# Optimization experiments

Measured on AMD Instinct MI355X. Metric: run time of the kernel, lower is better.

Reference implementation:

```python
import jax, jax.numpy as jnp
import numpy as np

NUM_HEAD = 8
HEAD_DIM = 32
MAX_DIST = 128
RATIO = 4  # smooth_embedding_ratio


def setup_inputs() -> dict:
    key = jax.random.key(0)
    ks = jax.random.split(key, 8)
    B, L, C = 4, 2048, 64
    H, D, md = NUM_HEAD, HEAD_DIM, MAX_DIST
    Wsm = (2 * md + 1) // RATIO  # 64

    def g(k, shape, scale=0.05):
        return jax.random.normal(k, shape, dtype=jnp.float32) * scale

    return {
        "x": g(ks[0], (B, L, C), 1.0),
        "Wq": g(ks[1], (C, H * D)),
        "bq": jnp.zeros((H * D,), jnp.float32),
        "Wk": g(ks[2], (C, H * D)),
        "bk": jnp.zeros((H * D,), jnp.float32),
        "Wv": g(ks[3], (C, H)),
        "distance_pe": g(ks[4], (H, D, Wsm, 1)),
        "u_pe": g(ks[5], (H, 1, 1, D)),
        "v_pe": g(ks[6], (H, 1, 1, D)),
    }


def reference(x, Wq, bq, Wk, bk, Wv, distance_pe, u_pe, v_pe):
    H, D, md = NUM_HEAD, HEAD_DIM, MAX_DIST
    W = 2 * md + 1
    B, L, _ = x.shape

    # projections, split into heads: (H, B, L, D)
    q = (x @ Wq + bq).reshape(B, L, H, D).transpose(2, 0, 1, 3)
    k = (x @ Wk + bk).reshape(B, L, H, D).transpose(2, 0, 1, 3)
    v = jax.nn.sigmoid(x @ Wv).transpose(2, 0, 1)  # (H, B, L)

    # Banded (q+u) @ k^T without materializing the full LxL score matrix.
    # TF does matmul + diag_part(k=(-md, md)) + permute + double reverse, which
    # equals att[h,b,n,m] = <q_u[h,b,(L-1-n)-(m-md)], k[h,b,L-1-n]> (0 if OOB).
    q_u = q + u_pe  # (H, B, L, D)
    q_pad = jnp.pad(q_u, ((0, 0), (0, 0), (md, md), (0, 0)))  # zeros match diag_part padding

    def band_at(m):
        # q_pad[j + 2*md - m] == q_u[j - (m - md)] (zero when out of range)
        qs = jax.lax.dynamic_slice_in_dim(q_pad, 2 * md - m, L, axis=2)
        return jnp.einsum('hbld,hbld->hbl', qs, k)

    band = jax.lax.map(band_at, jnp.arange(W))  # (W, H, B, L)
    att = jnp.transpose(band, (1, 2, 3, 0))[:, :, ::-1, :]  # (H, B, L, W)

    # Smoothed distance PE: bilinear upsample width Wsm -> W (TF2 half-pixel centers)
    smooth_pe = jax.image.resize(distance_pe, (H, D, W, 1), method='linear')[..., 0]  # (H, D, W)
    att = att + jnp.einsum('hbld,hdw->hblw', q + v_pe, smooth_pe)

    att = jax.nn.softmax(att * (float(D) ** -0.5), axis=-1)
    att = att * v[..., None]  # sigmoid value gating

    out = att.sum(axis=2)  # global mode: reduce over data_length -> (H, B, W)
    return jnp.transpose(out, (1, 2, 0))  # (B, W, H)
```

## Files before the change

kernel.cpp:

```cpp
#include <hip/hip_runtime.h>
#include <math.h>

#define NH 8
#define HD 32
#define MD 128
#define NW 257
#define NWP 272
#define WSM 64
#define NB 4
#define NL 2048
#define NC 64
#define NHD 256
#define SP 40
#define ROWS 128
#define WIN 384
#define WTS 72
#define TRS 136
#define SC2 0.2550928063161107f

#define NBLK 512

using bf16x8 = __attribute__((ext_vector_type(8))) short;
using f32x4  = __attribute__((ext_vector_type(4))) float;
using i32x4  = __attribute__((ext_vector_type(4))) int;

__device__ __forceinline__ unsigned cvtpk(float lo, float hi) {
  unsigned r;
  asm("v_cvt_pk_bf16_f32 %0, %1, %2" : "=v"(r) : "v"(lo), "v"(hi));
  return r;
}
__device__ __forceinline__ unsigned short f2b(float f) {
  return (unsigned short)cvtpk(f, f);
}
__device__ __forceinline__ void stb(unsigned short* p, float f) {
  *p = f2b(f);
}

__global__ __launch_bounds__(512, 4) void phaseA_kernel(
    const float* __restrict__ x,
    const float* __restrict__ Wq, const float* __restrict__ bq,
    const float* __restrict__ Wk, const float* __restrict__ bk,
    const float* __restrict__ Wv, const float* __restrict__ dpe,
    const float* __restrict__ u_pe,
    unsigned short* __restrict__ qu,
    unsigned short* __restrict__ kb, float* __restrict__ vv,
    unsigned short* __restrict__ spt, float* __restrict__ out) {
  __shared__ __align__(16) unsigned short wt[128 * WTS];
  __shared__ __align__(16) unsigned short tr[64 * TRS];
  const int bid = blockIdx.x;
  const int tid = threadIdx.x;

  bf16x8 a0, a1;
  int c = 0, g = 0, g8 = 0, w = 0, b = 0, l0 = 0, cb = 0;
  bool isQ = true;

  if (tid < 256) {
    const int t = tid;
    const int l64 = t & 63;
    w = t >> 6;
    c = l64 & 15; g = l64 >> 4; g8 = g * 8;
    const int br = bid >> 2;
    const int c0 = (bid & 3) << 7;
    const int r0 = br << 6;
    b = r0 >> 11;
    l0 = r0 & (NL - 1);
    isQ = (c0 < 256);
    const float* Wsrc = isQ ? Wq : Wk;
    cb = isQ ? c0 : c0 - 256;

#pragma unroll
    for (int i = 0; i < 4; ++i) {
      const int flat = t + i * 256;
      const int col4 = flat & 31;
      const int kp = flat >> 5;
      const float4 w0 = *reinterpret_cast<const float4*>(Wsrc + (2 * kp) * NHD + cb + 4 * col4);
      const float4 w1 = *reinterpret_cast<const float4*>(Wsrc + (2 * kp + 1) * NHD + cb + 4 * col4);
      unsigned* wp = reinterpret_cast<unsigned*>(wt);
      wp[(4 * col4 + 0) * (WTS / 2) + kp] = cvtpk(w0.x, w1.x);
      wp[(4 * col4 + 1) * (WTS / 2) + kp] = cvtpk(w0.y, w1.y);
      wp[(4 * col4 + 2) * (WTS / 2) + kp] = cvtpk(w0.z, w1.z);
      wp[(4 * col4 + 3) * (WTS / 2) + kp] = cvtpk(w0.w, w1.w);
    }

    const float* xr = x + (size_t)(r0 + 16 * w + c) * NC;
    const float4 x00 = *reinterpret_cast<const float4*>(xr + g8);
    const float4 x01 = *reinterpret_cast<const float4*>(xr + g8 + 4);
    const float4 x10 = *reinterpret_cast<const float4*>(xr + 32 + g8);
    const float4 x11 = *reinterpret_cast<const float4*>(xr + 32 + g8 + 4);
    const i32x4 a0i = {(int)cvtpk(x00.x, x00.y), (int)cvtpk(x00.z, x00.w),
                       (int)cvtpk(x01.x, x01.y), (int)cvtpk(x01.z, x01.w)};
    const i32x4 a1i = {(int)cvtpk(x10.x, x10.y), (int)cvtpk(x10.z, x10.w),
                       (int)cvtpk(x11.x, x11.y), (int)cvtpk(x11.z, x11.w)};
    a0 = __builtin_bit_cast(bf16x8, a0i);
    a1 = __builtin_bit_cast(bf16x8, a1i);
  } else if (tid < 384) {
    const int k = tid - 256;
    const int j = k >> 3, hh = k & 7;
    const int row = bid * 16 + j;
    const float* xr = x + (size_t)row * NC;
    float a = 0.f;
#pragma unroll
    for (int c4 = 0; c4 < NC / 4; ++c4) {
      const float4 xv = *reinterpret_cast<const float4*>(xr + 4 * c4);
      a = fmaf(xv.x, Wv[(4 * c4 + 0) * NH + hh], a);
      a = fmaf(xv.y, Wv[(4 * c4 + 1) * NH + hh], a);
      a = fmaf(xv.z, Wv[(4 * c4 + 2) * NH + hh], a);
      a = fmaf(xv.w, Wv[(4 * c4 + 3) * NH + hh], a);
    }
    const int bb = row >> 11, ll = row & (NL - 1);
    vv[((size_t)hh * NB + bb) * NL + ll] = 1.f / (1.f + __expf(-a));
  } else {
    const int k = tid - 384;
    if (k < 17) {
      const int oz = bid * 17 + k;
      if (oz < NB * NW * NH) out[oz] = 0.f;
    }
#pragma unroll
    for (int it = 0; it < 2; ++it) {
      const int k2 = k + it * 128;
      const int idx = bid * 136 + k2;
      if (k2 < 136 && idx < NH * NWP * HD) {
        const int d = idx & 31;
        const int hm = idx >> 5;
        const int m = hm % NWP;
        const int h = hm / NWP;
        float val = 0.f;
        if (m < NW) {
          float tt = (m + 0.5f) * ((float)WSM / (float)NW) - 0.5f;
          tt = fminf(fmaxf(tt, 0.f), (float)(WSM - 1));
          const int i0 = (int)tt;
          const float f = tt - (float)i0;
          const int i1 = (i0 + 1 < WSM) ? i0 + 1 : WSM - 1;
          const float* bse = dpe + ((size_t)h * HD + d) * WSM;
          val = (bse[i0] * (1.f - f) + bse[i1] * f) * SC2;
        }
        stb(spt + idx, val);
      }
    }
  }

  __syncthreads();

  if (tid < 256) {
    f32x4 acc[8];
#pragma unroll
    for (int tt = 0; tt < 8; ++tt) acc[tt] = {0.f, 0.f, 0.f, 0.f};
    __builtin_amdgcn_s_setprio(1);
#pragma unroll
    for (int tt = 0; tt < 8; ++tt) {
      const bf16x8 b0 = *reinterpret_cast<const bf16x8*>(&wt[(16 * tt + c) * WTS + g8]);
      const bf16x8 b1 = *reinterpret_cast<const bf16x8*>(&wt[(16 * tt + c) * WTS + 32 + g8]);
      acc[tt] = __builtin_amdgcn_mfma_f32_16x16x32_bf16(a0, b0, acc[tt], 0, 0, 0);
      acc[tt] = __builtin_amdgcn_mfma_f32_16x16x32_bf16(a1, b1, acc[tt], 0, 0, 0);
    }
    __builtin_amdgcn_s_setprio(0);
#pragma unroll
    for (int tt = 0; tt < 8; ++tt) {
      const int col = cb + 16 * tt + c;
      const float bias = isQ ? (bq[col] + u_pe[col]) : bk[col];
#pragma unroll
      for (int r = 0; r < 4; ++r) {
        const float val = isQ ? (acc[tt][r] + bias) : ((acc[tt][r] + bias) * SC2);
        tr[(16 * w + 4 * g + r) * TRS + 16 * tt + c] = f2b(val);
      }
    }
  }

  __syncthreads();

  if (tid < 256) {
    unsigned short* dst = isQ ? qu : kb;
#pragma unroll
    for (int i = 0; i < 4; ++i) {
      const int idx = tid + i * 256;
      const int row = idx >> 4;
      const int hd4 = (idx >> 2) & 3;
      const int ch = idx & 3;
      const i32x4 v = *reinterpret_cast<const i32x4*>(&tr[row * TRS + hd4 * 32 + ch * 8]);
      const int col0 = cb + hd4 * 32;
      const int h = col0 >> 5;
      *reinterpret_cast<i32x4*>(dst + (((size_t)h * NB + b) * NL + l0 + row) * HD + ch * 8) = v;
    }
  }
}

__global__ __launch_bounds__(512, 4) void phaseB_kernel(
    const unsigned short* __restrict__ qu,
    const unsigned short* __restrict__ kb, const float* __restrict__ vv,
    const unsigned short* __restrict__ spt,
    const float* __restrict__ u_pe, const float* __restrict__ v_pe,
    float* __restrict__ out) {
  __shared__ __align__(16) unsigned short qu_sh[WIN * SP];
  float* red = reinterpret_cast<float*>(qu_sh);

  const int raw = blockIdx.x;
  const int bid = (raw & 7) * 64 + (raw >> 3);
  const int tid = threadIdx.x;

  const int tile = bid & 15;
  const int hb = bid >> 4;
  const int b = hb & (NB - 1);
  const int h = hb >> 2;
  const int hc0 = h * HD;
  const int n0 = tile << 7;
  const int jlo = NL - ROWS - n0;
  const int l = tid & 63;
  const int w = tid >> 6;
  const int c = l & 15;
  const int g = l >> 4;
  const int g8 = g * 8;

  const unsigned short* qu_h = qu + (size_t)hb * NL * HD;
  const unsigned short* k_h  = kb + (size_t)hb * NL * HD;
  const unsigned short* sp_h = spt + (size_t)h * NWP * HD;
  const float* vv_h = vv + (size_t)hb * NL;

  const bf16x8 ak = *reinterpret_cast<const bf16x8*>(k_h + (size_t)(jlo + 16 * w + c) * HD + g8);
  const i32x4 qraw = *reinterpret_cast<const i32x4*>(qu_h + (size_t)(n0 + 127 - 16 * w - c) * HD + g8);
  const f32x4 v4 = *reinterpret_cast<const f32x4*>(vv_h + (n0 + 124 - 16 * w - 4 * g));

  const int wq0_blk = jlo - MD;
  i32x4 stq[3];
#pragma unroll
  for (int it = 0; it < 3; ++it) {
    const int p = tid + it * 512;
    const int gr = wq0_blk + (p >> 2);
    i32x4 val = {0, 0, 0, 0};
    if ((unsigned)gr < (unsigned)NL)
      val = *reinterpret_cast<const i32x4*>(qu_h + (size_t)gr * HD + (p & 3) * 8);
    stq[it] = val;
  }

  const float4 u0 = *reinterpret_cast<const float4*>(u_pe + hc0 + g8);
  const float4 u1 = *reinterpret_cast<const float4*>(u_pe + hc0 + g8 + 4);
  const float4 v0 = *reinterpret_cast<const float4*>(v_pe + hc0 + g8);
  const float4 v1 = *reinterpret_cast<const float4*>(v_pe + hc0 + g8 + 4);
  const float duv[8] = {v0.x - u0.x, v0.y - u0.y, v0.z - u0.z, v0.w - u0.w,
                        v1.x - u1.x, v1.y - u1.y, v1.z - u1.z, v1.w - u1.w};
  i32x4 aqv_i;
#pragma unroll
  for (int k2 = 0; k2 < 4; ++k2) {
    const unsigned uq = (unsigned)qraw[k2];
    const float lo = __builtin_bit_cast(float, uq << 16) + duv[2 * k2];
    const float hi = __builtin_bit_cast(float, uq & 0xffff0000u) + duv[2 * k2 + 1];
    aqv_i[k2] = (int)cvtpk(lo, hi);
  }
  const bf16x8 aqv = __builtin_bit_cast(bf16x8, aqv_i);

  const f32x4 z4 = {0.f, 0.f, 0.f, 0.f};

  f32x4 s[17];
  __builtin_amdgcn_s_setprio(1);
#pragma unroll
  for (int t = 0; t < 17; ++t) {
    const bf16x8 bsp = *reinterpret_cast<const bf16x8*>(sp_h + (size_t)(16 * t + c) * HD + g8);
    s[t] = __builtin_amdgcn_mfma_f32_16x16x32_bf16(aqv, bsp, z4, 0, 0, 0);
  }
  __builtin_amdgcn_s_setprio(0);

#pragma unroll
  for (int it = 0; it < 3; ++it) {
    const int p = tid + it * 512;
    *reinterpret_cast<i32x4*>(&qu_sh[(p >> 2) * SP + (p & 3) * 8]) = stq[it];
  }
  __syncthreads();

  int sl[4]; bool cond[4];
#pragma unroll
  for (int r = 0; r < 4; ++r) {
    sl[r] = 16 * g + ((4 * g + r - c) & 15);
    cond[r] = (4 * g + r) >= c;
  }

  f32x4 shp;
  __builtin_amdgcn_s_setprio(1);
#pragma unroll
  for (int U = 0; U <= 16; ++U) {
    const bf16x8 bqu = *reinterpret_cast<const bf16x8*>(&qu_sh[(16 * w + 16 * U + c) * SP + g8]);
    const f32x4 c1 = __builtin_amdgcn_mfma_f32_16x16x32_bf16(ak, bqu, z4, 0, 0, 0);
    f32x4 shc;
#pragma unroll
    for (int r = 0; r < 4; ++r) shc[r] = __shfl(c1[r], sl[r], 64);
    if (U == 0) {
#pragma unroll
      for (int r = 0; r < 4; ++r)
        s[16][r] = (c == 0) ? (s[16][r] + shc[r]) : -1e30f;
    } else {
#pragma unroll
      for (int r = 0; r < 4; ++r)
        s[16 - U][r] += cond[r] ? shc[r] : shp[r];
    }
    shp = shc;
  }
  __builtin_amdgcn_s_setprio(0);

  float wgt[4];
#pragma unroll
  for (int r = 0; r < 4; ++r) {
    float sum = 0.f;
#pragma unroll
    for (int t = 0; t < 17; ++t) {
      const float p = exp2f(s[t][r]);
      s[t][r] = p;
      sum += p;
    }
#pragma unroll
    for (int off = 1; off < 16; off <<= 1) sum += __shfl_xor(sum, off, 16);
    wgt[r] = v4[3 - r] * __builtin_amdgcn_rcpf(sum);
  }

  __syncthreads();
#pragma unroll
  for (int t = 0; t < 17; ++t) {
    float y = s[t][0] * wgt[0] + s[t][1] * wgt[1] + s[t][2] * wgt[2] + s[t][3] * wgt[3];
    y += __shfl_xor(y, 16, 64);
    y += __shfl_xor(y, 32, 64);
    if (l < 16) red[w * NWP + 16 * t + c] = y;
  }
  __syncthreads();
  for (int m = tid; m < NW; m += 512) {
    float ssum = 0.f;
#pragma unroll
    for (int ww = 0; ww < 8; ++ww) ssum += red[ww * NWP + m];
    atomicAdd(&out[((size_t)b * NW + m) * NH + h], ssum);
  }
}

extern "C" void kernel_launch(void* const* d_in, const int* in_sizes, int n_in,
                              void* d_out, int out_size, void* d_ws, size_t ws_size,
                              hipStream_t stream) {
  const float* x = (const float*)d_in[0];
  const float* Wq = (const float*)d_in[1];
  const float* bq = (const float*)d_in[2];
  const float* Wk = (const float*)d_in[3];
  const float* bk = (const float*)d_in[4];
  const float* Wv = (const float*)d_in[5];
  const float* dpe = (const float*)d_in[6];
  const float* u_pe = (const float*)d_in[7];
  const float* v_pe = (const float*)d_in[8];
  float* out = (float*)d_out;

  const size_t qk_elems = (size_t)NH * NB * NL * HD;
  float* vv = (float*)d_ws;
  unsigned short* qu = (unsigned short*)(vv + (size_t)NH * NB * NL);
  unsigned short* kb = qu + qk_elems;
  unsigned short* spt = kb + qk_elems;

  hipLaunchKernelGGL(phaseA_kernel, dim3(NBLK), dim3(512), 0, stream,
                     x, Wq, bq, Wk, bk, Wv, dpe, u_pe, qu, kb, vv, spt, out);
  hipLaunchKernelGGL(phaseB_kernel, dim3(NBLK), dim3(512), 0, stream,
                     qu, kb, vv, spt, u_pe, v_pe, out);
}
```

Measured before the change: 31.70 us.

## Fuse projection and band-attention phases into one kernel with grid barrier

Merges the two kernels into a single kernel. An atomic-counter grid-wide barrier separates the projection phase from the banded attention phase, and shared memory is aliased between the phases. This removes the second kernel launch and the gap between kernels. In exchange it adds a memset to reset the counter, and it relies on all 512 blocks being co-resident, or the spin barrier deadlocks.

After: 110.7 us. +249.1%, slower.

```diff
diff --git a/kernel.cpp b/kernel.cpp
--- a/kernel.cpp
+++ b/kernel.cpp
@@ -19,6 +19,7 @@
 #define SC2 0.2550928063161107f
 
 #define NBLK 512
+#define SMEM_U16 17920
 
 using bf16x8 = __attribute__((ext_vector_type(8))) short;
 using f32x4  = __attribute__((ext_vector_type(4))) float;
@@ -36,293 +37,301 @@
   *p = f2b(f);
 }
 
-__global__ __launch_bounds__(512, 4) void phaseA_kernel(
+__global__ __launch_bounds__(512, 4) void fused_kernel(
     const float* __restrict__ x,
     const float* __restrict__ Wq, const float* __restrict__ bq,
     const float* __restrict__ Wk, const float* __restrict__ bk,
     const float* __restrict__ Wv, const float* __restrict__ dpe,
-    const float* __restrict__ u_pe,
+    const float* __restrict__ u_pe, const float* __restrict__ v_pe,
     unsigned short* __restrict__ qu,
     unsigned short* __restrict__ kb, float* __restrict__ vv,
-    unsigned short* __restrict__ spt, float* __restrict__ out) {
-  __shared__ __align__(16) unsigned short wt[128 * WTS];
-  __shared__ __align__(16) unsigned short tr[64 * TRS];
-  const int bid = blockIdx.x;
+    unsigned short* __restrict__ spt, unsigned* __restrict__ ctr,
+    float* __restrict__ out) {
+  __shared__ __align__(16) unsigned short smem[SMEM_U16];
+  unsigned short* wt = smem;
+  unsigned short* tr = smem + 128 * WTS;
+  unsigned short* qu_sh = smem;
+  float* red = reinterpret_cast<float*>(smem);
+
+  const int rawbid = blockIdx.x;
   const int tid = threadIdx.x;
 
-  bf16x8 a0, a1;
-  int c = 0, g = 0, g8 = 0, w = 0, b = 0, l0 = 0, cb = 0;
-  bool isQ = true;
-
-  if (tid < 256) {
-    const int t = tid;
-    const int l64 = t & 63;
-    w = t >> 6;
-    c = l64 & 15; g = l64 >> 4; g8 = g * 8;
-    const int br = bid >> 2;
-    const int c0 = (bid & 3) << 7;
-    const int r0 = br << 6;
-    b = r0 >> 11;
-    l0 = r0 & (NL - 1);
-    isQ = (c0 < 256);
-    const float* Wsrc = isQ ? Wq : Wk;
-    cb = isQ ? c0 : c0 - 256;
-
-#pragma unroll
-    for (int i = 0; i < 4; ++i) {
-      const int flat = t + i * 256;
-      const int col4 = flat & 31;
-      const int kp = flat >> 5;
-      const float4 w0 = *reinterpret_cast<const float4*>(Wsrc + (2 * kp) * NHD + cb + 4 * col4);
-      const float4 w1 = *reinterpret_cast<const float4*>(Wsrc + (2 * kp + 1) * NHD + cb + 4 * col4);
-      unsigned* wp = reinterpret_cast<unsigned*>(wt);
-      wp[(4 * col4 + 0) * (WTS / 2) + kp] = cvtpk(w0.x, w1.x);
-      wp[(4 * col4 + 1) * (WTS / 2) + kp] = cvtpk(w0.y, w1.y);
-      wp[(4 * col4 + 2) * (WTS / 2) + kp] = cvtpk(w0.z, w1.z);
-      wp[(4 * col4 + 3) * (WTS / 2) + kp] = cvtpk(w0.w, w1.w);
-    }
-
-    const float* xr = x + (size_t)(r0 + 16 * w + c) * NC;
-    const float4 x00 = *reinterpret_cast<const float4*>(xr + g8);
-    const float4 x01 = *reinterpret_cast<const float4*>(xr + g8 + 4);
-    const float4 x10 = *reinterpret_cast<const float4*>(xr + 32 + g8);
-    const float4 x11 = *reinterpret_cast<const float4*>(xr + 32 + g8 + 4);
-    const i32x4 a0i = {(int)cvtpk(x00.x, x00.y), (int)cvtpk(x00.z, x00.w),
-                       (int)cvtpk(x01.x, x01.y), (int)cvtpk(x01.z, x01.w)};
-    const i32x4 a1i = {(int)cvtpk(x10.x, x10.y), (int)cvtpk(x10.z, x10.w),
-                       (int)cvtpk(x11.x, x11.y), (int)cvtpk(x11.z, x11.w)};
-    a0 = __builtin_bit_cast(bf16x8, a0i);
-    a1 = __builtin_bit_cast(bf16x8, a1i);
-  } else if (tid < 384) {
-    const int k = tid - 256;
-    const int j = k >> 3, hh = k & 7;
-    const int row = bid * 16 + j;
-    const float* xr = x + (size_t)row * NC;
-    float a = 0.f;
-#pragma unroll
-    for (int c4 = 0; c4 < NC / 4; ++c4) {
-      const float4 xv = *reinterpret_cast<const float4*>(xr + 4 * c4);
-      a = fmaf(xv.x, Wv[(4 * c4 + 0) * NH + hh], a);
-      a = fmaf(xv.y, Wv[(4 * c4 + 1) * NH + hh], a);
-      a = fmaf(xv.z, Wv[(4 * c4 + 2) * NH + hh], a);
-      a = fmaf(xv.w, Wv[(4 * c4 + 3) * NH + hh], a);
-    }
-    const int bb = row >> 11, ll = row & (NL - 1);
-    vv[((size_t)hh * NB + bb) * NL + ll] = 1.f / (1.f + __expf(-a));
-  } else {
-    const int k = tid - 384;
-    if (k < 17) {
-      const int oz = bid * 17 + k;
-      if (oz < NB * NW * NH) out[oz] = 0.f;
-    }
-#pragma unroll
-    for (int it = 0; it < 2; ++it) {
-      const int k2 = k + it * 128;
-      const int idx = bid * 136 + k2;
-      if (k2 < 136 && idx < NH * NWP * HD) {
-        const int d = idx & 31;
-        const int hm = idx >> 5;
-        const int m = hm % NWP;
-        const int h = hm / NWP;
-        float val = 0.f;
-        if (m < NW) {
-          float tt = (m + 0.5f) * ((float)WSM / (float)NW) - 0.5f;
-          tt = fminf(fmaxf(tt, 0.f), (float)(WSM - 1));
-          const int i0 = (int)tt;
-          const float f = tt - (float)i0;
-          const int i1 = (i0 + 1 < WSM) ? i0 + 1 : WSM - 1;
-          const float* bse = dpe + ((size_t)h * HD + d) * WSM;
-          val = (bse[i0] * (1.f - f) + bse[i1] * f) * SC2;
+  {
+    const int bid = rawbid;
+    bf16x8 a0, a1;
+    int c = 0, g = 0, g8 = 0, w = 0, b = 0, l0 = 0, cb = 0;
+    bool isQ = true;
+
+    if (tid < 256) {
+      const int t = tid;
+      const int l64 = t & 63;
+      w = t >> 6;
+      c = l64 & 15; g = l64 >> 4; g8 = g * 8;
+      const int br = bid >> 2;
+      const int c0 = (bid & 3) << 7;
+      const int r0 = br << 6;
+      b = r0 >> 11;
+      l0 = r0 & (NL - 1);
+      isQ = (c0 < 256);
+      const float* Wsrc = isQ ? Wq : Wk;
+      cb = isQ ? c0 : c0 - 256;
+
+#pragma unroll
+      for (int i = 0; i < 4; ++i) {
+        const int flat = t + i * 256;
+        const int col4 = flat & 31;
+        const int kp = flat >> 5;
+        const float4 w0 = *reinterpret_cast<const float4*>(Wsrc + (2 * kp) * NHD + cb + 4 * col4);
+        const float4 w1 = *reinterpret_cast<const float4*>(Wsrc + (2 * kp + 1) * NHD + cb + 4 * col4);
+        unsigned* wp = reinterpret_cast<unsigned*>(wt);
+        wp[(4 * col4 + 0) * (WTS / 2) + kp] = cvtpk(w0.x, w1.x);
+        wp[(4 * col4 + 1) * (WTS / 2) + kp] = cvtpk(w0.y, w1.y);
+        wp[(4 * col4 + 2) * (WTS / 2) + kp] = cvtpk(w0.z, w1.z);
+        wp[(4 * col4 + 3) * (WTS / 2) + kp] = cvtpk(w0.w, w1.w);
+      }
+
+      const float* xr = x + (size_t)(r0 + 16 * w + c) * NC;
+      const float4 x00 = *reinterpret_cast<const float4*>(xr + g8);
+      const float4 x01 = *reinterpret_cast<const float4*>(xr + g8 + 4);
+      const float4 x10 = *reinterpret_cast<const float4*>(xr + 32 + g8);
+      const float4 x11 = *reinterpret_cast<const float4*>(xr + 32 + g8 + 4);
+      const i32x4 a0i = {(int)cvtpk(x00.x, x00.y), (int)cvtpk(x00.z, x00.w),
+                         (int)cvtpk(x01.x, x01.y), (int)cvtpk(x01.z, x01.w)};
+      const i32x4 a1i = {(int)cvtpk(x10.x, x10.y), (int)cvtpk(x10.z, x10.w),
+                         (int)cvtpk(x11.x, x11.y), (int)cvtpk(x11.z, x11.w)};
+      a0 = __builtin_bit_cast(bf16x8, a0i);
+      a1 = __builtin_bit_cast(bf16x8, a1i);
+    } else if (tid < 384) {
+      const int k = tid - 256;
+      const int j = k >> 3, hh = k & 7;
+      const int row = bid * 16 + j;
+      const float* xr = x + (size_t)row * NC;
+      float a = 0.f;
+#pragma unroll
+      for (int c4 = 0; c4 < NC / 4; ++c4) {
+        const float4 xv = *reinterpret_cast<const float4*>(xr + 4 * c4);
+        a = fmaf(xv.x, Wv[(4 * c4 + 0) * NH + hh], a);
+        a = fmaf(xv.y, Wv[(4 * c4 + 1) * NH + hh], a);
+        a = fmaf(xv.z, Wv[(4 * c4 + 2) * NH + hh], a);
+        a = fmaf(xv.w, Wv[(4 * c4 + 3) * NH + hh], a);
+      }
+      const int bb = row >> 11, ll = row & (NL - 1);
+      vv[((size_t)hh * NB + bb) * NL + ll] = 1.f / (1.f + __expf(-a));
+    } else {
+      const int k = tid - 384;
+      if (k < 17) {
+        const int oz = bid * 17 + k;
+        if (oz < NB * NW * NH) out[oz] = 0.f;
+      }
+#pragma unroll
+      for (int it = 0; it < 2; ++it) {
+        const int k2 = k + it * 128;
+        const int idx = bid * 136 + k2;
+        if (k2 < 136 && idx < NH * NWP * HD) {
+          const int d = idx & 31;
+          const int hm = idx >> 5;
+          const int m = hm % NWP;
+          const int h = hm / NWP;
+          float val = 0.f;
+          if (m < NW) {
+            float tt = (m + 0.5f) * ((float)WSM / (float)NW) - 0.5f;
+            tt = fminf(fmaxf(tt, 0.f), (float)(WSM - 1));
+            const int i0 = (int)tt;
+            const float f = tt - (float)i0;
+            const int i1 = (i0 + 1 < WSM) ? i0 + 1 : WSM - 1;
+            const float* bse = dpe + ((size_t)h * HD + d) * WSM;
+            val = (bse[i0] * (1.f - f) + bse[i1] * f) * SC2;
+          }
+          stb(spt + idx, val);
         }
-        stb(spt + idx, val);
+      }
+    }
+
+    __syncthreads();
+
+    if (tid < 256) {
+      f32x4 acc[8];
+#pragma unroll
+      for (int tt = 0; tt < 8; ++tt) acc[tt] = {0.f, 0.f, 0.f, 0.f};
+      __builtin_amdgcn_s_setprio(1);
+#pragma unroll
+      for (int tt = 0; tt < 8; ++tt) {
+        const bf16x8 b0 = *reinterpret_cast<const bf16x8*>(&wt[(16 * tt + c) * WTS + g8]);
+        const bf16x8 b1 = *reinterpret_cast<const bf16x8*>(&wt[(16 * tt + c) * WTS + 32 + g8]);
+        acc[tt] = __builtin_amdgcn_mfma_f32_16x16x32_bf16(a0, b0, acc[tt], 0, 0, 0);
+        acc[tt] = __builtin_amdgcn_mfma_f32_16x16x32_bf16(a1, b1, acc[tt], 0, 0, 0);
+      }
+      __builtin_amdgcn_s_setprio(0);
+#pragma unroll
+      for (int tt = 0; tt < 8; ++tt) {
+        const int col = cb + 16 * tt + c;
+        const float bias = isQ ? (bq[col] + u_pe[col]) : bk[col];
+#pragma unroll
+        for (int r = 0; r < 4; ++r) {
+          const float val = isQ ? (acc[tt][r] + bias) : ((acc[tt][r] + bias) * SC2);
+          tr[(16 * w + 4 * g + r) * TRS + 16 * tt + c] = f2b(val);
+        }
+      }
+    }
+
+    __syncthreads();
+
+    if (tid < 256) {
+      unsigned short* dst = isQ ? qu : kb;
+#pragma unroll
+      for (int i = 0; i < 4; ++i) {
+        const int idx = tid + i * 256;
+        const int row = idx >> 4;
+        const int hd4 = (idx >> 2) & 3;
+        const int ch = idx & 3;
+        const i32x4 v = *reinterpret_cast<const i32x4*>(&tr[row * TRS + hd4 * 32 + ch * 8]);
+        const int col0 = cb + hd4 * 32;
+        const int h = col0 >> 5;
+        *reinterpret_cast<i32x4*>(dst + (((size_t)h * NB + b) * NL + l0 + row) * HD + ch * 8) = v;
       }
     }
   }
 
   __syncthreads();
-
-  if (tid < 256) {
-    f32x4 acc[8];
-#pragma unroll
-    for (int tt = 0; tt < 8; ++tt) acc[tt] = {0.f, 0.f, 0.f, 0.f};
-    __builtin_amdgcn_s_setprio(1);
-#pragma unroll
-    for (int tt = 0; tt < 8; ++tt) {
-      const bf16x8 b0 = *reinterpret_cast<const bf16x8*>(&wt[(16 * tt + c) * WTS + g8]);
-      const bf16x8 b1 = *reinterpret_cast<const bf16x8*>(&wt[(16 * tt + c) * WTS + 32 + g8]);
-      acc[tt] = __builtin_amdgcn_mfma_f32_16x16x32_bf16(a0, b0, acc[tt], 0, 0, 0);
-      acc[tt] = __builtin_amdgcn_mfma_f32_16x16x32_bf16(a1, b1, acc[tt], 0, 0, 0);
-    }
-    __builtin_amdgcn_s_setprio(0);
-#pragma unroll
-    for (int tt = 0; tt < 8; ++tt) {
-      const int col = cb + 16 * tt + c;
-      const float bias = isQ ? (bq[col] + u_pe[col]) : bk[col];
-#pragma unroll
-      for (int r = 0; r < 4; ++r) {
-        const float val = isQ ? (acc[tt][r] + bias) : ((acc[tt][r] + bias) * SC2);
-        tr[(16 * w + 4 * g + r) * TRS + 16 * tt + c] = f2b(val);
-      }
-    }
-  }
-
-  __syncthreads();
-
-  if (tid < 256) {
-    unsigned short* dst = isQ ? qu : kb;
-#pragma unroll
-    for (int i = 0; i < 4; ++i) {
-      const int idx = tid + i * 256;
-      const int row = idx >> 4;
-      const int hd4 = (idx >> 2) & 3;
-      const int ch = idx & 3;
-      const i32x4 v = *reinterpret_cast<const i32x4*>(&tr[row * TRS + hd4 * 32 + ch * 8]);
-      const int col0 = cb + hd4 * 32;
-      const int h = col0 >> 5;
-      *reinterpret_cast<i32x4*>(dst + (((size_t)h * NB + b) * NL + l0 + row) * HD + ch * 8) = v;
-    }
-  }
-}
-
-__global__ __launch_bounds__(512, 4) void phaseB_kernel(
-    const unsigned short* __restrict__ qu,
-    const unsigned short* __restrict__ kb, const float* __restrict__ vv,
-    const unsigned short* __restrict__ spt,
-    const float* __restrict__ u_pe, const float* __restrict__ v_pe,
-    float* __restrict__ out) {
-  __shared__ __align__(16) unsigned short qu_sh[WIN * SP];
-  float* red = reinterpret_cast<float*>(qu_sh);
-
-  const int raw = blockIdx.x;
-  const int bid = (raw & 7) * 64 + (raw >> 3);
-  const int tid = threadIdx.x;
-
-  const int tile = bid & 15;
-  const int hb = bid >> 4;
-  const int b = hb & (NB - 1);
-  const int h = hb >> 2;
-  const int hc0 = h * HD;
-  const int n0 = tile << 7;
-  const int jlo = NL - ROWS - n0;
-  const int l = tid & 63;
-  const int w = tid >> 6;
-  const int c = l & 15;
-  const int g = l >> 4;
-  const int g8 = g * 8;
-
-  const unsigned short* qu_h = qu + (size_t)hb * NL * HD;
-  const unsigned short* k_h  = kb + (size_t)hb * NL * HD;
-  const unsigned short* sp_h = spt + (size_t)h * NWP * HD;
-  const float* vv_h = vv + (size_t)hb * NL;
-
-  const bf16x8 ak = *reinterpret_cast<const bf16x8*>(k_h + (size_t)(jlo + 16 * w + c) * HD + g8);
-  const i32x4 qraw = *reinterpret_cast<const i32x4*>(qu_h + (size_t)(n0 + 127 - 16 * w - c) * HD + g8);
-  const f32x4 v4 = *reinterpret_cast<const f32x4*>(vv_h + (n0 + 124 - 16 * w - 4 * g));
-
-  const int wq0_blk = jlo - MD;
-  i32x4 stq[3];
-#pragma unroll
-  for (int it = 0; it < 3; ++it) {
-    const int p = tid + it * 512;
-    const int gr = wq0_blk + (p >> 2);
-    i32x4 val = {0, 0, 0, 0};
-    if ((unsigned)gr < (unsigned)NL)
-      val = *reinterpret_cast<const i32x4*>(qu_h + (size_t)gr * HD + (p & 3) * 8);
-    stq[it] = val;
-  }
-
-  const float4 u0 = *reinterpret_cast<const float4*>(u_pe + hc0 + g8);
-  const float4 u1 = *reinterpret_cast<const float4*>(u_pe + hc0 + g8 + 4);
-  const float4 v0 = *reinterpret_cast<const float4*>(v_pe + hc0 + g8);
-  const float4 v1 = *reinterpret_cast<const float4*>(v_pe + hc0 + g8 + 4);
-  const float duv[8] = {v0.x - u0.x, v0.y - u0.y, v0.z - u0.z, v0.w - u0.w,
-                        v1.x - u1.x, v1.y - u1.y, v1.z - u1.z, v1.w - u1.w};
-  i32x4 aqv_i;
-#pragma unroll
-  for (int k2 = 0; k2 < 4; ++k2) {
-    const unsigned uq = (unsigned)qraw[k2];
-    const float lo = __builtin_bit_cast(float, uq << 16) + duv[2 * k2];
-    const float hi = __builtin_bit_cast(float, uq & 0xffff0000u) + duv[2 * k2 + 1];
-    aqv_i[k2] = (int)cvtpk(lo, hi);
-  }
-  const bf16x8 aqv = __builtin_bit_cast(bf16x8, aqv_i);
-
-  const f32x4 z4 = {0.f, 0.f, 0.f, 0.f};
-
-  f32x4 s[17];
-  __builtin_amdgcn_s_setprio(1);
-#pragma unroll
-  for (int t = 0; t < 17; ++t) {
-    const bf16x8 bsp = *reinterpret_cast<const bf16x8*>(sp_h + (size_t)(16 * t + c) * HD + g8);
-    s[t] = __builtin_amdgcn_mfma_f32_16x16x32_bf16(aqv, bsp, z4, 0, 0, 0);
-  }
-  __builtin_amdgcn_s_setprio(0);
-
-#pragma unroll
-  for (int it = 0; it < 3; ++it) {
-    const int p = tid + it * 512;
-    *reinterpret_cast<i32x4*>(&qu_sh[(p >> 2) * SP + (p & 3) * 8]) = stq[it];
+  if (tid == 0) {
+    __threadfence();
+    __hip_atomic_fetch_add(ctr, 1u, __ATOMIC_ACQ_REL, __HIP_MEMORY_SCOPE_AGENT);
+    while (__hip_atomic_load(ctr, __ATOMIC_ACQUIRE, __HIP_MEMORY_SCOPE_AGENT) < (unsigned)NBLK)
+      __builtin_amdgcn_s_sleep(8);
+    __threadfence();
   }
   __syncthreads();
 
-  int sl[4]; bool cond[4];
-#pragma unroll
-  for (int r = 0; r < 4; ++r) {
-    sl[r] = 16 * g + ((4 * g + r - c) & 15);
-    cond[r] = (4 * g + r) >= c;
-  }
-
-  f32x4 shp;
-  __builtin_amdgcn_s_setprio(1);
-#pragma unroll
-  for (int U = 0; U <= 16; ++U) {
-    const bf16x8 bqu = *reinterpret_cast<const bf16x8*>(&qu_sh[(16 * w + 16 * U + c) * SP + g8]);
-    const f32x4 c1 = __builtin_amdgcn_mfma_f32_16x16x32_bf16(ak, bqu, z4, 0, 0, 0);
-    f32x4 shc;
-#pragma unroll
-    for (int r = 0; r < 4; ++r) shc[r] = __shfl(c1[r], sl[r], 64);
-    if (U == 0) {
-#pragma unroll
-      for (int r = 0; r < 4; ++r)
-        s[16][r] = (c == 0) ? (s[16][r] + shc[r]) : -1e30f;
-    } else {
-#pragma unroll
-      for (int r = 0; r < 4; ++r)
-        s[16 - U][r] += cond[r] ? shc[r] : shp[r];
-    }
-    shp = shc;
-  }
-  __builtin_amdgcn_s_setprio(0);
-
-  float wgt[4];
-#pragma unroll
-  for (int r = 0; r < 4; ++r) {
-    float sum = 0.f;
+  {
+    const int bid = (rawbid & 7) * 64 + (rawbid >> 3);
+
+    const int tile = bid & 15;
+    const int hb = bid >> 4;
+    const int b = hb & (NB - 1);
+    const int h = hb >> 2;
+    const int hc0 = h * HD;
+    const int n0 = tile << 7;
+    const int jlo = NL - ROWS - n0;
+    const int l = tid & 63;
+    const int w = tid >> 6;
+    const int c = l & 15;
+    const int g = l >> 4;
+    const int g8 = g * 8;
+
+    const unsigned short* qu_h = qu + (size_t)hb * NL * HD;
+    const unsigned short* k_h  = kb + (size_t)hb * NL * HD;
+    const unsigned short* sp_h = spt + (size_t)h * NWP * HD;
+    const float* vv_h = vv + (size_t)hb * NL;
+
+    const bf16x8 ak = *reinterpret_cast<const bf16x8*>(k_h + (size_t)(jlo + 16 * w + c) * HD + g8);
+    const i32x4 qraw = *reinterpret_cast<const i32x4*>(qu_h + (size_t)(n0 + 127 - 16 * w - c) * HD + g8);
+    const f32x4 v4 = *reinterpret_cast<const f32x4*>(vv_h + (n0 + 124 - 16 * w - 4 * g));
+
+    const int wq0_blk = jlo - MD;
+    i32x4 stq[3];
+#pragma unroll
+    for (int it = 0; it < 3; ++it) {
+      const int p = tid + it * 512;
+      const int gr = wq0_blk + (p >> 2);
+      i32x4 val = {0, 0, 0, 0};
+      if ((unsigned)gr < (unsigned)NL)
+        val = *reinterpret_cast<const i32x4*>(qu_h + (size_t)gr * HD + (p & 3) * 8);
+      stq[it] = val;
+    }
+
+    const float4 u0 = *reinterpret_cast<const float4*>(u_pe + hc0 + g8);
+    const float4 u1 = *reinterpret_cast<const float4*>(u_pe + hc0 + g8 + 4);
+    const float4 v0 = *reinterpret_cast<const float4*>(v_pe + hc0 + g8);
+    const float4 v1 = *reinterpret_cast<const float4*>(v_pe + hc0 + g8 + 4);
+    const float duv[8] = {v0.x - u0.x, v0.y - u0.y, v0.z - u0.z, v0.w - u0.w,
+                          v1.x - u1.x, v1.y - u1.y, v1.z - u1.z, v1.w - u1.w};
+    i32x4 aqv_i;
+#pragma unroll
+    for (int k2 = 0; k2 < 4; ++k2) {
+      const unsigned uq = (unsigned)qraw[k2];
+      const float lo = __builtin_bit_cast(float, uq << 16) + duv[2 * k2];
+      const float hi = __builtin_bit_cast(float, uq & 0xffff0000u) + duv[2 * k2 + 1];
+      aqv_i[k2] = (int)cvtpk(lo, hi);
+    }
+    const bf16x8 aqv = __builtin_bit_cast(bf16x8, aqv_i);
+
+    const f32x4 z4 = {0.f, 0.f, 0.f, 0.f};
+
+    f32x4 s[17];
+    __builtin_amdgcn_s_setprio(1);
 #pragma unroll
     for (int t = 0; t < 17; ++t) {
-      const float p = exp2f(s[t][r]);
-      s[t][r] = p;
-      sum += p;
-    }
-#pragma unroll
-    for (int off = 1; off < 16; off <<= 1) sum += __shfl_xor(sum, off, 16);
-    wgt[r] = v4[3 - r] * __builtin_amdgcn_rcpf(sum);
-  }
-
-  __syncthreads();
-#pragma unroll
-  for (int t = 0; t < 17; ++t) {
-    float y = s[t][0] * wgt[0] + s[t][1] * wgt[1] + s[t][2] * wgt[2] + s[t][3] * wgt[3];
-    y += __shfl_xor(y, 16, 64);
-    y += __shfl_xor(y, 32, 64);
-    if (l < 16) red[w * NWP + 16 * t + c] = y;
-  }
-  __syncthreads();
-  for (int m = tid; m < NW; m += 512) {
-    float ssum = 0.f;
-#pragma unroll
-    for (int ww = 0; ww < 8; ++ww) ssum += red[ww * NWP + m];
-    atomicAdd(&out[((size_t)b * NW + m) * NH + h], ssum);
+      const bf16x8 bsp = *reinterpret_cast<const bf16x8*>(sp_h + (size_t)(16 * t + c) * HD + g8);
+      s[t] = __builtin_amdgcn_mfma_f32_16x16x32_bf16(aqv, bsp, z4, 0, 0, 0);
+    }
+    __builtin_amdgcn_s_setprio(0);
+
+#pragma unroll
+    for (int it = 0; it < 3; ++it) {
+      const int p = tid + it * 512;
+      *reinterpret_cast<i32x4*>(&qu_sh[(p >> 2) * SP + (p & 3) * 8]) = stq[it];
+    }
+    __syncthreads();
+
+    int sl[4]; bool cond[4];
+#pragma unroll
+    for (int r = 0; r < 4; ++r) {
+      sl[r] = 16 * g + ((4 * g + r - c) & 15);
+      cond[r] = (4 * g + r) >= c;
+    }
+
+    f32x4 shp;
+    __builtin_amdgcn_s_setprio(1);
+#pragma unroll
+    for (int U = 0; U <= 16; ++U) {
+      const bf16x8 bqu = *reinterpret_cast<const bf16x8*>(&qu_sh[(16 * w + 16 * U + c) * SP + g8]);
+      const f32x4 c1 = __builtin_amdgcn_mfma_f32_16x16x32_bf16(ak, bqu, z4, 0, 0, 0);
+      f32x4 shc;
+#pragma unroll
+      for (int r = 0; r < 4; ++r) shc[r] = __shfl(c1[r], sl[r], 64);
+      if (U == 0) {
+#pragma unroll
+        for (int r = 0; r < 4; ++r)
+          s[16][r] = (c == 0) ? (s[16][r] + shc[r]) : -1e30f;
+      } else {
+#pragma unroll
+        for (int r = 0; r < 4; ++r)
+          s[16 - U][r] += cond[r] ? shc[r] : shp[r];
+      }
+      shp = shc;
+    }
+    __builtin_amdgcn_s_setprio(0);
+
+    float wgt[4];
+#pragma unroll
+    for (int r = 0; r < 4; ++r) {
+      float sum = 0.f;
+#pragma unroll
+      for (int t = 0; t < 17; ++t) {
+        const float p = exp2f(s[t][r]);
+        s[t][r] = p;
+        sum += p;
+      }
+#pragma unroll
+      for (int off = 1; off < 16; off <<= 1) sum += __shfl_xor(sum, off, 16);
+      wgt[r] = v4[3 - r] * __builtin_amdgcn_rcpf(sum);
+    }
+
+    __syncthreads();
+#pragma unroll
+    for (int t = 0; t < 17; ++t) {
+      float y = s[t][0] * wgt[0] + s[t][1] * wgt[1] + s[t][2] * wgt[2] + s[t][3] * wgt[3];
+      y += __shfl_xor(y, 16, 64);
+      y += __shfl_xor(y, 32, 64);
+      if (l < 16) red[w * NWP + 16 * t + c] = y;
+    }
+    __syncthreads();
+    for (int m = tid; m < NW; m += 512) {
+      float ssum = 0.f;
+#pragma unroll
+      for (int ww = 0; ww < 8; ++ww) ssum += red[ww * NWP + m];
+      atomicAdd(&out[((size_t)b * NW + m) * NH + h], ssum);
+    }
   }
 }
 
@@ -341,13 +350,13 @@
   float* out = (float*)d_out;
 
   const size_t qk_elems = (size_t)NH * NB * NL * HD;
-  float* vv = (float*)d_ws;
+  unsigned* ctr = (unsigned*)d_ws;
+  float* vv = (float*)d_ws + 16;
   unsigned short* qu = (unsigned short*)(vv + (size_t)NH * NB * NL);
   unsigned short* kb = qu + qk_elems;
   unsigned short* spt = kb + qk_elems;
 
-  hipLaunchKernelGGL(phaseA_kernel, dim3(NBLK), dim3(512), 0, stream,
-                     x, Wq, bq, Wk, bk, Wv, dpe, u_pe, qu, kb, vv, spt, out);
-  hipLaunchKernelGGL(phaseB_kernel, dim3(NBLK), dim3(512), 0, stream,
-                     qu, kb, vv, spt, u_pe, v_pe, out);
-}
+  hipMemsetAsync(ctr, 0, sizeof(unsigned), stream);
+  hipLaunchKernelGGL(fused_kernel, dim3(NBLK), dim3(512), 0, stream,
+                     x, Wq, bq, Wk, bk, Wv, dpe, u_pe, v_pe, qu, kb, vv, spt, ctr, out);
+}
```
